# Optimization experiments

Hardware: AMD Instinct MI355X
Metric: run time of the kernel (lower is better)

Reference implementation:

```python
import jax, jax.numpy as jnp
import numpy as np
from jax import lax

D_MODEL, D_STATE, D_CONV, D_INNER, DT_RANK = 1024, 16, 4, 2048, 64
B_SZ, L_SEQ = 2, 4096

def setup_inputs() -> dict:
    key = jax.random.key(0)
    ks = jax.random.split(key, 12)
    s = 0.02
    x = jax.random.normal(ks[0], (B_SZ, L_SEQ, D_MODEL), jnp.float32)
    norm_w = jnp.ones((D_MODEL,), jnp.float32)
    norm_b = jnp.zeros((D_MODEL,), jnp.float32)
    W_in = jax.random.normal(ks[1], (D_MODEL, 2 * D_INNER), jnp.float32) * s
    conv_w = jax.random.normal(ks[2], (D_INNER, 1, D_CONV), jnp.float32) * 0.5
    conv_b = jnp.zeros((D_INNER,), jnp.float32)
    W_x = jax.random.normal(ks[3], (D_INNER, DT_RANK + 2 * D_STATE), jnp.float32) * s
    W_dt = jax.random.normal(ks[4], (DT_RANK, D_INNER), jnp.float32) * s
    # dt bias init as in the torch module: inverse-softplus of dt in [dt_min, dt_max]
    dt_init = jnp.exp(jax.random.uniform(ks[5], (D_INNER,)) * (np.log(0.1) - np.log(0.001)) + np.log(0.001))
    dt_init = jnp.clip(dt_init, 1e-4, None)
    b_dt = dt_init + jnp.log(-jnp.expm1(-dt_init))
    A_log = jnp.log(jnp.broadcast_to(jnp.arange(1, D_STATE + 1, dtype=jnp.float32)[None, :], (D_INNER, D_STATE)))
    D = jnp.ones((D_INNER,), jnp.float32)
    W_out = jax.random.normal(ks[6], (D_INNER, D_MODEL), jnp.float32) * s
    return {"x": x, "norm_w": norm_w, "norm_b": norm_b, "W_in": W_in,
            "conv_w": conv_w, "conv_b": conv_b, "W_x": W_x, "W_dt": W_dt,
            "b_dt": b_dt, "A_log": A_log, "D": D, "W_out": W_out}

def _silu(v):
    return v * jax.nn.sigmoid(v)

def _layernorm(v, w, b, eps=1e-5):
    mu = jnp.mean(v, axis=-1, keepdims=True)
    var = jnp.var(v, axis=-1, keepdims=True)
    return (v - mu) * lax.rsqrt(var + eps) * w + b

def _selective_scan(u, delta, A, Bm, Cm, Dp):
    # u, delta: [B,L,d_inner]; A: [d_inner,N]; Bm, Cm: [B,L,N]; Dp: [d_inner]
    Bb, L, d_inner = u.shape
    N = A.shape[1]

    def step(h, inp):
        dt_t, u_t, B_t, C_t = inp  # [B,d_inner],[B,d_inner],[B,N],[B,N]
        A_bar = jnp.exp(dt_t[..., None] * A)                       # [B,d_inner,N]
        h = A_bar * h + dt_t[..., None] * B_t[:, None, :] * u_t[..., None]
        y = jnp.sum(h * C_t[:, None, :], axis=-1)                  # [B,d_inner]
        return h, y

    h0 = jnp.zeros((Bb, d_inner, N), u.dtype)
    xs = (jnp.swapaxes(delta, 0, 1), jnp.swapaxes(u, 0, 1),
          jnp.swapaxes(Bm, 0, 1), jnp.swapaxes(Cm, 0, 1))
    _, ys = lax.scan(step, h0, xs)          # ys: [L,B,d_inner]
    y = jnp.swapaxes(ys, 0, 1)
    return y + u * Dp[None, None, :]

def reference(x, norm_w, norm_b, W_in, conv_w, conv_b, W_x, W_dt, b_dt, A_log, D, W_out):
    residual = x
    xn = _layernorm(x, norm_w, norm_b)
    xz = xn @ W_in                                      # [B,L,2*d_inner]
    x_ssm, z = jnp.split(xz, 2, axis=-1)
    # depthwise causal conv1d (torch pads both sides then truncates -> left pad)
    xt = jnp.swapaxes(x_ssm, 1, 2)                      # [B,d_inner,L]
    xt = jnp.pad(xt, ((0, 0), (0, 0), (D_CONV - 1, 0)))
    xc = lax.conv_general_dilated(xt, conv_w, window_strides=(1,), padding='VALID',
                                  feature_group_count=D_INNER,
                                  dimension_numbers=('NCH', 'OIH', 'NCH'))
    xc = xc + conv_b[None, :, None]
    x_conv = jnp.swapaxes(_silu(xc), 1, 2)              # [B,L,d_inner]
    x_dbl = x_conv @ W_x                                # [B,L,dt_rank+2N]
    dt_low, B_mat, C_mat = jnp.split(x_dbl, [DT_RANK, DT_RANK + D_STATE], axis=-1)
    delta = jax.nn.softplus(dt_low @ W_dt + b_dt)       # [B,L,d_inner]
    A = -jnp.exp(A_log)
    y = _selective_scan(x_conv, delta, A, B_mat, C_mat, D)
    y = y * _silu(z)
    return residual + y @ W_out
```

## Files before the change

kernel.cpp:

```cpp
#include <hip/hip_runtime.h>

typedef unsigned short u16;
typedef __attribute__((ext_vector_type(8))) __bf16 bf16x8;
typedef __attribute__((ext_vector_type(4))) float f32x4;

#define LSEQ 4096
#define DMODEL 1024
#define DINNER 2048

__device__ __forceinline__ float bf2f(u16 u) {
  union { unsigned u; float f; } v; v.u = ((unsigned)u) << 16; return v.f;
}
__device__ __forceinline__ u16 f2bf(float f) {
  union { float f; unsigned u; } v; v.f = f;
  unsigned r = v.u + 0x7fffu + ((v.u >> 16) & 1u);
  return (u16)(r >> 16);
}
__device__ __forceinline__ void gload_lds16(const void* g, void* l) {
  __builtin_amdgcn_global_load_lds(
      (__attribute__((address_space(1))) void*)(unsigned long long)g,
      (__attribute__((address_space(3))) void*)(unsigned int)(unsigned long long)l,
      16, 0, 0);
}
__device__ __forceinline__ float sigmoidf_(float v) { return 1.f / (1.f + __expf(-v)); }

__device__ __forceinline__ void swz_block(int gx, int& bn, int& bm) {
  int lin = blockIdx.x + gridDim.x * blockIdx.y;
  int q = (gridDim.x * gridDim.y) >> 3;
  int s = (lin & 7) * q + (lin >> 3);
  bn = s % gx;
  bm = s / gx;
}

#define SBAR { __builtin_amdgcn_s_barrier(); __builtin_amdgcn_sched_barrier(0); }

__global__ __launch_bounds__(256) void ln_kernel(const float* __restrict__ x,
                                                 const float* __restrict__ w,
                                                 const float* __restrict__ b,
                                                 u16* __restrict__ out) {
  int row = blockIdx.x;
  const float* xr = x + (size_t)row * DMODEL;
  int t = threadIdx.x;
  float4 v = ((const float4*)xr)[t];
  float s = v.x + v.y + v.z + v.w;
  float s2 = v.x * v.x + v.y * v.y + v.z * v.z + v.w * v.w;
  for (int off = 32; off; off >>= 1) {
    s += __shfl_down(s, off);
    s2 += __shfl_down(s2, off);
  }
  __shared__ float ls[4], ls2[4];
  int wid = t >> 6;
  if ((t & 63) == 0) { ls[wid] = s; ls2[wid] = s2; }
  __syncthreads();
  s = ls[0] + ls[1] + ls[2] + ls[3];
  s2 = ls2[0] + ls2[1] + ls2[2] + ls2[3];
  float mu = s * (1.f / DMODEL);
  float var = s2 * (1.f / DMODEL) - mu * mu;
  float rs = rsqrtf(var + 1e-5f);
  float4 wv = ((const float4*)w)[t];
  float4 bv = ((const float4*)b)[t];
  unsigned p0 = (unsigned)f2bf((v.x - mu) * rs * wv.x + bv.x) |
                ((unsigned)f2bf((v.y - mu) * rs * wv.y + bv.y) << 16);
  unsigned p1 = (unsigned)f2bf((v.z - mu) * rs * wv.z + bv.z) |
                ((unsigned)f2bf((v.w - mu) * rs * wv.w + bv.w) << 16);
  ((uint2*)(out + (size_t)row * DMODEL))[t] = make_uint2(p0, p1);
}

__global__ __launch_bounds__(256) void tc_all(const float* __restrict__ W_in,
                                              const float* __restrict__ W_x,
                                              const float* __restrict__ W_dt,
                                              const float* __restrict__ W_out,
                                              u16* __restrict__ o0, u16* __restrict__ o1,
                                              u16* __restrict__ o2, u16* __restrict__ o3) {
  __shared__ float tile[32][33];
  int id = blockIdx.x;
  const float* in;
  u16* out;
  int K, N, Npad, gx, bx;
  if (id < 4096)      { in = W_in;  out = o0; K = 1024; N = 4096; Npad = 4096; gx = 128; bx = id; }
  else if (id < 4352) { in = W_x;   out = o1; K = 2048; N = 96;   Npad = 128;  gx = 4;   bx = id - 4096; }
  else if (id < 4480) { in = W_dt;  out = o2; K = 64;   N = 2048; Npad = 2048; gx = 64;  bx = id - 4352; }
  else                { in = W_out; out = o3; K = 2048; N = 1024; Npad = 1024; gx = 32;  bx = id - 4480; }
  int n0 = (bx % gx) * 32, k0 = (bx / gx) * 32;
  int tx = threadIdx.x & 31, ty = threadIdx.x >> 5;
  for (int i = ty; i < 32; i += 8) {
    int k = k0 + i, n = n0 + tx;
    tile[i][tx] = (k < K && n < N) ? in[(size_t)k * N + n] : 0.f;
  }
  __syncthreads();
  for (int i = ty; i < 32; i += 8) {
    int n = n0 + i, k = k0 + tx;
    if (n < Npad && k < K) out[(size_t)n * K + k] = f2bf(tile[tx][i]);
  }
}

__device__ __forceinline__ void stage8(const u16* grow0, int ld, int kcol0,
                                       u16* lds_u, int ln) {
  int rr = ln >> 3, kb = ln & 7;
  gload_lds16(grow0 + (size_t)rr * ld + kcol0 + ((kb ^ rr) << 3), lds_u);
}

#define LDA_F(mh, BUF)                                                             \
  _Pragma("unroll") for (int mf = 0; mf < 4; ++mf) {                               \
    av[mf][0] = *(const bf16x8*)(qA0 + (BUF) * 16384 + ((mh) * 64 + mf * 16) * 64); \
    av[mf][1] = *(const bf16x8*)(qA1 + (BUF) * 16384 + ((mh) * 64 + mf * 16) * 64); \
  }

#define LDB_F(nh, BUF)                                                             \
  _Pragma("unroll") for (int nf = 0; nf < 2; ++nf) {                               \
    bb[nh][nf][0] = *(const bf16x8*)(qB0 + (BUF) * 16384 + ((nh) * 32 + nf * 16) * 64); \
    bb[nh][nf][1] = *(const bf16x8*)(qB1 + (BUF) * 16384 + ((nh) * 32 + nf * 16) * 64); \
  }

#define MFMA_Q(mh, nh)                                                             \
  __builtin_amdgcn_s_setprio(1);                                                   \
  _Pragma("unroll") for (int mf = 0; mf < 4; ++mf)                                 \
  _Pragma("unroll") for (int nf = 0; nf < 2; ++nf)                                 \
  _Pragma("unroll") for (int kk = 0; kk < 2; ++kk)                                 \
    acc[(mh) * 4 + mf][(nh) * 2 + nf] = __builtin_amdgcn_mfma_f32_16x16x32_bf16(   \
        av[mf][kk], bb[nh][nf][kk], acc[(mh) * 4 + mf][(nh) * 2 + nf], 0, 0, 0);   \
  __builtin_amdgcn_s_setprio(0);

#define STAGE_A(unit, kt, buf)                                                     \
  _Pragma("unroll") for (int c = 0; c < 2; ++c) {                                  \
    int g = w * 2 + c;                                                             \
    int r0 = ((g < 8) ? g * 8 : (g - 8) * 8 + 128) + (unit) * 64;                  \
    stage8(Ag + (size_t)r0 * ldK, ldK, (kt) * 64, LA + (buf) * 16384 + r0 * 64, ln); \
  }

#define STAGE_B(half, kt, buf)                                                     \
  _Pragma("unroll") for (int c = 0; c < 2; ++c) {                                  \
    int g = w * 2 + c;                                                             \
    int r0 = (g >> 2) * 64 + (half) * 32 + (g & 3) * 8;                            \
    stage8(Bg + (size_t)r0 * ldK, ldK, (kt) * 64, LB + (buf) * 16384 + r0 * 64, ln); \
  }

#define PHASES8P(T_, B0_, B1_)                                                     \
  {                                                                                \
    int kt1 = ((T_) + 1 < NT) ? (T_) + 1 : NT - 1;                                 \
    int kt2 = ((T_) + 2 < NT) ? (T_) + 2 : NT - 1;                                 \
    LDA_F(0, B0_); LDB_F(0, B0_);                                                  \
    STAGE_A(1, kt1, B1_);                                                          \
    MFMA_Q(0, 0);                                                                  \
    SBAR                                                                           \
    LDB_F(1, B0_);                                                                 \
    STAGE_A(0, kt2, B0_);                                                          \
    MFMA_Q(0, 1);                                                                  \
    SBAR                                                                           \
    LDA_F(1, B0_);                                                                 \
    STAGE_B(0, kt2, B0_);                                                          \
    MFMA_Q(1, 1);                                                                  \
    SBAR                                                                           \
    STAGE_B(1, kt2, B0_);                                                          \
    asm volatile("s_waitcnt vmcnt(6)" ::: "memory");                               \
    MFMA_Q(1, 0);                                                                  \
    SBAR                                                                           \
  }

template <int OUT_BF16, int EPI>
__global__ __launch_bounds__(512, 2) void gemm8p(const u16* __restrict__ A,
                                                 const u16* __restrict__ Bt,
                                                 void* __restrict__ Cout,
                                                 const float* __restrict__ aux,
                                                 int M, int N, int K, int cthresh) {
  __shared__ alignas(16) u16 lds[65536];
  u16* LA = lds;
  u16* LB = lds + 32768;
  int t = threadIdx.x;
  int w = t >> 6, ln = t & 63;
  int wm = w >> 2, wn = w & 3;
  int bn, bm;
  swz_block(gridDim.x, bn, bm);
  int lr = ln & 15, lq = ln >> 4, key = ln & 7;
  int ldK = K;
  int NT = K >> 6;
  const u16* Ag = A + (size_t)bm * 256 * ldK;
  const u16* Bg = Bt + (size_t)bn * 256 * ldK;
  const u16* qA0 = LA + (wm * 128 + lr) * 64 + ((lq ^ key) << 3);
  const u16* qA1 = LA + (wm * 128 + lr) * 64 + (((4 + lq) ^ key) << 3);
  const u16* qB0 = LB + (wn * 64 + lr) * 64 + ((lq ^ key) << 3);
  const u16* qB1 = LB + (wn * 64 + lr) * 64 + (((4 + lq) ^ key) << 3);
  f32x4 acc[8][4] = {};
  bf16x8 av[4][2], bb[2][2][2];

  STAGE_A(0, 0, 0); STAGE_B(0, 0, 0); STAGE_B(1, 0, 0); STAGE_A(1, 0, 0);
  int k1 = NT > 1 ? 1 : 0;
  STAGE_A(0, k1, 1); STAGE_B(0, k1, 1); STAGE_B(1, k1, 1);
  asm volatile("s_waitcnt vmcnt(6)" ::: "memory");
  SBAR

  for (int TT = 0; TT < NT; TT += 2) {
    PHASES8P(TT, 0, 1)
    PHASES8P(TT + 1, 1, 0)
  }

  int crow0 = bm * 256 + wm * 128;
  int ccol0 = bn * 256 + wn * 64;
#pragma unroll
  for (int mf = 0; mf < 8; ++mf)
#pragma unroll
    for (int nf = 0; nf < 4; ++nf)
#pragma unroll
      for (int r = 0; r < 4; ++r) {
        int row = crow0 + mf * 16 + lq * 4 + r;
        int col = ccol0 + nf * 16 + lr;
        float v = acc[mf][nf][r];
        if (EPI == 1) v += aux[(size_t)row * N + col];
        if (EPI == 2 && col >= cthresh) v = v * sigmoidf_(v);
        if (OUT_BF16)
          ((u16*)Cout)[(size_t)row * N + col] = f2bf(v);
        else
          ((float*)Cout)[(size_t)row * N + col] = v;
      }
}

#define LDA128(mh, BUF)                                                            \
  _Pragma("unroll") for (int mf2 = 0; mf2 < 2; ++mf2) {                            \
    av[mf2][0] = *(const bf16x8*)(rA0 + (BUF) * 8192 + ((mh) * 32 + mf2 * 16) * 64); \
    av[mf2][1] = *(const bf16x8*)(rA1 + (BUF) * 8192 + ((mh) * 32 + mf2 * 16) * 64); \
  }

#define LDB128(nh, BUF, B_)                                                        \
  _Pragma("unroll") for (int nf2 = 0; nf2 < 2; ++nf2) {                            \
    B_[nf2][0] = *(const bf16x8*)(rB0 + (BUF) * 16384 + ((nh) * 32 + nf2 * 16) * 64); \
    B_[nf2][1] = *(const bf16x8*)(rB1 + (BUF) * 16384 + ((nh) * 32 + nf2 * 16) * 64); \
  }

#define MFMA_Q128(mh, nh, B_)                                                      \
  __builtin_amdgcn_s_setprio(1);                                                   \
  _Pragma("unroll") for (int mf2 = 0; mf2 < 2; ++mf2)                              \
  _Pragma("unroll") for (int nf2 = 0; nf2 < 2; ++nf2)                              \
  _Pragma("unroll") for (int kk = 0; kk < 2; ++kk)                                 \
    acc[(mh) * 2 + mf2][(nh) * 2 + nf2] = __builtin_amdgcn_mfma_f32_16x16x32_bf16( \
        av[mf2][kk], B_[nf2][kk], acc[(mh) * 2 + mf2][(nh) * 2 + nf2], 0, 0, 0);   \
  __builtin_amdgcn_s_setprio(0);

#define STAGE_A128(unit, kt, buf)                                                  \
  {                                                                                \
    int r0 = (w >> 2) * 64 + (unit) * 32 + (w & 3) * 8;                            \
    stage8(Ag + (size_t)r0 * ldK, ldK, (kt) * 64, LA + (buf) * 8192 + r0 * 64, ln); \
  }

#define STAGE_B128(half, kt, buf)                                                  \
  _Pragma("unroll") for (int c = 0; c < 2; ++c) {                                  \
    int g = w * 2 + c;                                                             \
    int r0 = (g >> 2) * 64 + (half) * 32 + (g & 3) * 8;                            \
    stage8(Bg + (size_t)r0 * ldK, ldK, (kt) * 64, LB + (buf) * 16384 + r0 * 64, ln); \
  }

#define PHASES128(T_, B0_, B1_)                                                    \
  {                                                                                \
    int kt1 = ((T_) + 1 < NT) ? (T_) + 1 : NT - 1;                                 \
    int kt2 = ((T_) + 2 < NT) ? (T_) + 2 : NT - 1;                                 \
    LDA128(0, B0_);                                                                \
    LDB128(0, B0_, bbl);                                                           \
    STAGE_A128(1, kt1, B1_);                                                       \
    MFMA_Q128(0, 0, bbl);                                                          \
    SBAR                                                                           \
    LDB128(1, B0_, bbh);                                                           \
    STAGE_A128(0, kt2, B0_);                                                       \
    MFMA_Q128(0, 1, bbh);                                                          \
    SBAR                                                                           \
    LDA128(1, B0_);                                                                \
    STAGE_B128(0, kt2, B0_);                                                       \
    MFMA_Q128(1, 1, bbh);                                                          \
    SBAR                                                                           \
    STAGE_B128(1, kt2, B0_);                                                       \
    asm volatile("s_waitcnt vmcnt(5)" ::: "memory");                               \
    MFMA_Q128(1, 0, bbl);                                                          \
    SBAR                                                                           \
  }

__global__ __launch_bounds__(512, 2) void gemm128_res(const u16* __restrict__ A,
                                                      const u16* __restrict__ Bt,
                                                      float* __restrict__ Cout,
                                                      const float* __restrict__ res,
                                                      int M, int N, int K) {
  __shared__ alignas(16) u16 lds[49152];
  u16* LA = lds;
  u16* LB = lds + 16384;
  int t = threadIdx.x;
  int w = t >> 6, ln = t & 63;
  int wm = w >> 2, wn = w & 3;
  int bn, bm;
  swz_block(gridDim.x, bn, bm);
  int lr = ln & 15, lq = ln >> 4, key = ln & 7;
  int ldK = K;
  int NT = K >> 6;
  const u16* Ag = A + (size_t)bm * 128 * ldK;
  const u16* Bg = Bt + (size_t)bn * 256 * ldK;
  const u16* rA0 = LA + (wm * 64 + lr) * 64 + ((lq ^ key) << 3);
  const u16* rA1 = LA + (wm * 64 + lr) * 64 + (((4 + lq) ^ key) << 3);
  const u16* rB0 = LB + (wn * 64 + lr) * 64 + ((lq ^ key) << 3);
  const u16* rB1 = LB + (wn * 64 + lr) * 64 + (((4 + lq) ^ key) << 3);
  f32x4 acc[4][4] = {};
  bf16x8 av[2][2], bbl[2][2], bbh[2][2];

  STAGE_A128(0, 0, 0); STAGE_B128(0, 0, 0); STAGE_B128(1, 0, 0); STAGE_A128(1, 0, 0);
  int k1 = NT > 1 ? 1 : 0;
  STAGE_A128(0, k1, 1); STAGE_B128(0, k1, 1); STAGE_B128(1, k1, 1);
  asm volatile("s_waitcnt vmcnt(5)" ::: "memory");
  SBAR

  for (int TT = 0; TT < NT; TT += 2) {
    PHASES128(TT, 0, 1)
    PHASES128(TT + 1, 1, 0)
  }

  int crow0 = bm * 128 + wm * 64;
  int ccol0 = bn * 256 + wn * 64;
#pragma unroll
  for (int mf = 0; mf < 4; ++mf)
#pragma unroll
    for (int nf = 0; nf < 4; ++nf)
#pragma unroll
      for (int r = 0; r < 4; ++r) {
        int row = crow0 + mf * 16 + lq * 4 + r;
        int col = ccol0 + nf * 16 + lr;
        Cout[(size_t)row * N + col] = acc[mf][nf][r] + res[(size_t)row * N + col];
      }
}

template <int OUT_BF16, int EPI, int SPLITK>
__global__ __launch_bounds__(256) void gemm_bt(const u16* __restrict__ A,
                                               const u16* __restrict__ Bt,
                                               void* __restrict__ Cout,
                                               const float* __restrict__ aux,
                                               int M, int N, int K, int ld, int cthresh) {
  __shared__ alignas(16) u16 As[128 * 32];
  __shared__ alignas(16) u16 Bs[128 * 32];
  int t = threadIdx.x;
  int w = t >> 6, ln = t & 63;
  int wr = w >> 1, wc = w & 1;
  int bm = blockIdx.y, bn = blockIdx.x;
  int lr = ln & 15, lk = (ln >> 4) * 8;
  f32x4 acc[4][4] = {};
  int kz = SPLITK ? blockIdx.z * K : 0;
  const u16* Abase = A + (size_t)bm * 128 * ld + kz;
  const u16* Bbase = Bt + (size_t)bn * 128 * ld + kz;
  for (int k0 = 0; k0 < K; k0 += 32) {
#pragma unroll
    for (int c = 0; c < 2; ++c) {
      int chunk = w * 2 + c;
      int ee = chunk * 512 + ln * 8;
      int row = ee >> 5, col = ee & 31;
      gload_lds16(Abase + (size_t)row * ld + k0 + col, As + chunk * 512);
      gload_lds16(Bbase + (size_t)row * ld + k0 + col, Bs + chunk * 512);
    }
    __syncthreads();
    bf16x8 af[4], bfr[4];
#pragma unroll
    for (int m = 0; m < 4; ++m)
      af[m] = *(const bf16x8*)(As + (wr * 64 + m * 16 + lr) * 32 + lk);
#pragma unroll
    for (int n = 0; n < 4; ++n)
      bfr[n] = *(const bf16x8*)(Bs + (wc * 64 + n * 16 + lr) * 32 + lk);
#pragma unroll
    for (int m = 0; m < 4; ++m)
#pragma unroll
      for (int n = 0; n < 4; ++n)
        acc[m][n] = __builtin_amdgcn_mfma_f32_16x16x32_bf16(af[m], bfr[n], acc[m][n], 0, 0, 0);
    __syncthreads();
  }
  int rb = bm * 128 + wr * 64 + (ln >> 4) * 4;
  int cb = bn * 128 + wc * 64 + lr;
  float* Cpart = SPLITK ? ((float*)Cout + (size_t)blockIdx.z * M * N) : (float*)Cout;
#pragma unroll
  for (int m = 0; m < 4; ++m)
#pragma unroll
    for (int n = 0; n < 4; ++n)
#pragma unroll
      for (int r = 0; r < 4; ++r) {
        int row = rb + m * 16 + r;
        int col = cb + n * 16;
        float v = acc[m][n][r];
        if (EPI == 3) {
          float dtr = v + aux[col];
          v = dtr > 15.f ? dtr : __logf(1.f + __expf(dtr));
        }
        if (OUT_BF16)
          ((u16*)Cpart)[(size_t)row * N + col] = f2bf(v);
        else
          Cpart[(size_t)row * N + col] = v;
      }
}

__global__ __launch_bounds__(256) void reduce_xdbl(const float* __restrict__ part,
                                                   float* __restrict__ xdbl,
                                                   u16* __restrict__ dtlow) {
  int i = blockIdx.x * 256 + threadIdx.x;
  float s = 0.f;
#pragma unroll
  for (int z = 0; z < 8; ++z) s += part[(size_t)z * (8192 * 128) + i];
  xdbl[i] = s;
  int col = i & 127;
  if (col < 64) dtlow[(size_t)(i >> 7) * 64 + col] = f2bf(s);
}

__global__ __launch_bounds__(256) void conv_silu(const u16* __restrict__ xz,
                                                 const float* __restrict__ cw,
                                                 const float* __restrict__ cb,
                                                 u16* __restrict__ out) {
  int d2 = blockIdx.x * 256 + threadIdx.x;
  int d = d2 * 2;
  int l0 = blockIdx.y * 8;
  int b = blockIdx.z;
  float w0a = cw[d * 4 + 0], w1a = cw[d * 4 + 1], w2a = cw[d * 4 + 2], w3a = cw[d * 4 + 3];
  float w0b = cw[d * 4 + 4], w1b = cw[d * 4 + 5], w2b = cw[d * 4 + 6], w3b = cw[d * 4 + 7];
  float biasa = cb[d], biasb = cb[d + 1];
  const u16* xp = xz + ((size_t)b * LSEQ) * 4096 + d;
  float xa[11], xb[11];
#pragma unroll
  for (int i = 0; i < 11; ++i) {
    int l = l0 - 3 + i;
    unsigned pk = (l >= 0) ? *(const unsigned*)(xp + (size_t)l * 4096) : 0u;
    xa[i] = bf2f((u16)(pk & 0xffffu));
    xb[i] = bf2f((u16)(pk >> 16));
  }
  u16* op = out + ((size_t)b * LSEQ + l0) * DINNER + d;
#pragma unroll
  for (int i = 0; i < 8; ++i) {
    float va = biasa + w0a * xa[i] + w1a * xa[i + 1] + w2a * xa[i + 2] + w3a * xa[i + 3];
    float vb = biasb + w0b * xb[i] + w1b * xb[i + 1] + w2b * xb[i + 2] + w3b * xb[i + 3];
    unsigned pk = (unsigned)f2bf(va * sigmoidf_(va)) |
                  ((unsigned)f2bf(vb * sigmoidf_(vb)) << 16);
    *(unsigned*)(op + (size_t)i * DINNER) = pk;
  }
}

__device__ __forceinline__ void compute_a(float dt, const float* An, bool fast, float* av) {
  if (fast) {
    float q = __expf(-dt);
    float q2 = q * q, q4 = q2 * q2;
    av[0] = q; av[1] = q2; av[2] = q2 * q; av[3] = q4;
#pragma unroll
    for (int n = 4; n < 16; ++n) av[n] = av[n - 4] * q4;
  } else {
#pragma unroll
    for (int n = 0; n < 16; ++n) av[n] = __expf(dt * An[n]);
  }
}

__device__ __forceinline__ void load_An(const float* A_log, int d, float* An, bool& fast) {
  const float4* A4 = (const float4*)(A_log + (size_t)d * 16);
  fast = true;
#pragma unroll
  for (int q = 0; q < 4; ++q) {
    float4 a = A4[q];
    An[q * 4 + 0] = -__expf(a.x);
    An[q * 4 + 1] = -__expf(a.y);
    An[q * 4 + 2] = -__expf(a.z);
    An[q * 4 + 3] = -__expf(a.w);
  }
#pragma unroll
  for (int n = 0; n < 16; ++n)
    fast = fast && (__builtin_fabsf(An[n] + (float)(n + 1)) < 1e-3f * (n + 1));
}

__global__ __launch_bounds__(256) void scan1(const u16* __restrict__ dtbf,
                                             const u16* __restrict__ ubf,
                                             const float* __restrict__ xdbl,
                                             const float* __restrict__ A_log,
                                             float* __restrict__ P,
                                             float* __restrict__ H) {
  int d = blockIdx.x * 256 + threadIdx.x;
  int b = blockIdx.y, c = blockIdx.z;
  size_t row0 = (size_t)b * LSEQ + c * 64;
  float An[16];
  bool fast;
  load_An(A_log, d, An, fast);
  const u16* dtp = dtbf + row0 * DINNER + d;
  const u16* up = ubf + row0 * DINNER + d;
  const float* Bp = xdbl + row0 * 128 + 64;
  float h[16];
#pragma unroll
  for (int n = 0; n < 16; ++n) h[n] = 0.f;
  float sdt = 0.f;
  float dt_c = bf2f(dtp[0]);
  float uu_c = bf2f(up[0]);
  const float4* B4 = (const float4*)Bp;
  float4 b0c = B4[0], b1c = B4[1], b2c = B4[2], b3c = B4[3];
  for (int i = 0; i < 64; ++i) {
    float dt_n = dt_c, uu_n = uu_c;
    float4 b0n = b0c, b1n = b1c, b2n = b2c, b3n = b3c;
    if (i < 63) {
      dt_n = bf2f(dtp[(size_t)(i + 1) * DINNER]);
      uu_n = bf2f(up[(size_t)(i + 1) * DINNER]);
      const float4* B4n = (const float4*)(Bp + (size_t)(i + 1) * 128);
      b0n = B4n[0]; b1n = B4n[1]; b2n = B4n[2]; b3n = B4n[3];
    }
    float dtu = dt_c * uu_c;
    sdt += dt_c;
    float Bf[16] = {b0c.x, b0c.y, b0c.z, b0c.w, b1c.x, b1c.y, b1c.z, b1c.w,
                    b2c.x, b2c.y, b2c.z, b2c.w, b3c.x, b3c.y, b3c.z, b3c.w};
    float av[16];
    compute_a(dt_c, An, fast, av);
#pragma unroll
    for (int n = 0; n < 16; ++n) h[n] = av[n] * h[n] + dtu * Bf[n];
    dt_c = dt_n; uu_c = uu_n;
    b0c = b0n; b1c = b1n; b2c = b2n; b3c = b3n;
  }
  size_t idx = (size_t)c * 65536 + ((size_t)b * DINNER + d) * 16;
  float4* P4 = (float4*)(P + idx);
  float4* H4 = (float4*)(H + idx);
#pragma unroll
  for (int q = 0; q < 4; ++q) {
    P4[q] = make_float4(__expf(An[q * 4 + 0] * sdt), __expf(An[q * 4 + 1] * sdt),
                        __expf(An[q * 4 + 2] * sdt), __expf(An[q * 4 + 3] * sdt));
    H4[q] = make_float4(h[q * 4], h[q * 4 + 1], h[q * 4 + 2], h[q * 4 + 3]);
  }
}

__global__ __launch_bounds__(256) void scan2(const float* __restrict__ P,
                                             const float* __restrict__ H,
                                             float* __restrict__ Hinit) {
  int i = blockIdx.x * 256 + threadIdx.x;
  float h = 0.f;
  for (int c = 0; c < 64; ++c) {
    Hinit[(size_t)c * 65536 + i] = h;
    h = P[(size_t)c * 65536 + i] * h + H[(size_t)c * 65536 + i];
  }
}

__global__ __launch_bounds__(256) void scan3(const u16* __restrict__ dtbf,
                                             const u16* __restrict__ ubf,
                                             const float* __restrict__ xdbl,
                                             const float* __restrict__ A_log,
                                             const float* __restrict__ Dp,
                                             const u16* __restrict__ xzbf,
                                             const float* __restrict__ Hinit,
                                             u16* __restrict__ ybf) {
  int d = blockIdx.x * 256 + threadIdx.x;
  int b = blockIdx.y, c = blockIdx.z;
  size_t row0 = (size_t)b * LSEQ + c * 64;
  float An[16];
  bool fast;
  load_An(A_log, d, An, fast);
  const u16* dtp = dtbf + row0 * DINNER + d;
  const u16* up = ubf + row0 * DINNER + d;
  const float* Bp = xdbl + row0 * 128 + 64;
  const float* Cp = xdbl + row0 * 128 + 80;
  const u16* gp = xzbf + row0 * 4096 + DINNER + d;
  u16* yp = ybf + row0 * DINNER + d;
  float Dv = Dp[d];
  float h[16];
  {
    const float4* Hi4 = (const float4*)(Hinit + (size_t)c * 65536 + ((size_t)b * DINNER + d) * 16);
#pragma unroll
    for (int q = 0; q < 4; ++q) {
      float4 hv = Hi4[q];
      h[q * 4 + 0] = hv.x; h[q * 4 + 1] = hv.y; h[q * 4 + 2] = hv.z; h[q * 4 + 3] = hv.w;
    }
  }
  float dt_c = bf2f(dtp[0]);
  float uu_c = bf2f(up[0]);
  float g_c = bf2f(gp[0]);
  const float4* B4 = (const float4*)Bp;
  const float4* C4 = (const float4*)Cp;
  float4 b0c = B4[0], b1c = B4[1], b2c = B4[2], b3c = B4[3];
  float4 c0c = C4[0], c1c = C4[1], c2c = C4[2], c3c = C4[3];
  for (int i = 0; i < 64; ++i) {
    float dt_n = dt_c, uu_n = uu_c, g_n = g_c;
    float4 b0n = b0c, b1n = b1c, b2n = b2c, b3n = b3c;
    float4 c0n = c0c, c1n = c1c, c2n = c2c, c3n = c3c;
    if (i < 63) {
      dt_n = bf2f(dtp[(size_t)(i + 1) * DINNER]);
      uu_n = bf2f(up[(size_t)(i + 1) * DINNER]);
      g_n = bf2f(gp[(size_t)(i + 1) * 4096]);
      const float4* B4n = (const float4*)(Bp + (size_t)(i + 1) * 128);
      const float4* C4n = (const float4*)(Cp + (size_t)(i + 1) * 128);
      b0n = B4n[0]; b1n = B4n[1]; b2n = B4n[2]; b3n = B4n[3];
      c0n = C4n[0]; c1n = C4n[1]; c2n = C4n[2]; c3n = C4n[3];
    }
    float dtu = dt_c * uu_c;
    float Bf[16] = {b0c.x, b0c.y, b0c.z, b0c.w, b1c.x, b1c.y, b1c.z, b1c.w,
                    b2c.x, b2c.y, b2c.z, b2c.w, b3c.x, b3c.y, b3c.z, b3c.w};
    float Cf[16] = {c0c.x, c0c.y, c0c.z, c0c.w, c1c.x, c1c.y, c1c.z, c1c.w,
                    c2c.x, c2c.y, c2c.z, c2c.w, c3c.x, c3c.y, c3c.z, c3c.w};
    float av[16];
    compute_a(dt_c, An, fast, av);
    float y = 0.f;
#pragma unroll
    for (int n = 0; n < 16; ++n) {
      h[n] = av[n] * h[n] + dtu * Bf[n];
      y += h[n] * Cf[n];
    }
    yp[(size_t)i * DINNER] = f2bf((y + uu_c * Dv) * g_c);
    dt_c = dt_n; uu_c = uu_n; g_c = g_n;
    b0c = b0n; b1c = b1n; b2c = b2n; b3c = b3n;
    c0c = c0n; c1c = c1n; c2c = c2n; c3c = c3n;
  }
}

extern "C" void kernel_launch(void* const* d_in, const int* in_sizes, int n_in,
                              void* d_out, int out_size, void* d_ws, size_t ws_size,
                              hipStream_t stream) {
  const float* x = (const float*)d_in[0];
  const float* nw = (const float*)d_in[1];
  const float* nb = (const float*)d_in[2];
  const float* W_in = (const float*)d_in[3];
  const float* convw = (const float*)d_in[4];
  const float* convb = (const float*)d_in[5];
  const float* W_x = (const float*)d_in[6];
  const float* W_dt = (const float*)d_in[7];
  const float* b_dt = (const float*)d_in[8];
  const float* A_log = (const float*)d_in[9];
  const float* Dp = (const float*)d_in[10];
  const float* W_out = (const float*)d_in[11];
  float* out = (float*)d_out;

  char* wp = (char*)d_ws;
  auto alloc = [&](size_t bytes) {
    char* p = wp;
    wp += (bytes + 255) & ~(size_t)255;
    return p;
  };
  u16* xz_bf = (u16*)alloc((size_t)8192 * 4096 * 2);
  u16* xconv_bf = (u16*)alloc((size_t)8192 * 2048 * 2);
  u16* xn_bf = (u16*)alloc((size_t)8192 * 1024 * 2);
  float* xdbl = (float*)alloc((size_t)8192 * 128 * 4);
  u16* dt_bf = (u16*)alloc((size_t)8192 * 2048 * 2);
  u16* dtlow_bf = (u16*)alloc((size_t)8192 * 64 * 2);
  u16* Wint = (u16*)alloc((size_t)4096 * 1024 * 2);
  u16* Wxt = (u16*)alloc((size_t)128 * 2048 * 2);
  u16* Wdtt = (u16*)alloc((size_t)2048 * 64 * 2);
  u16* Woutt = (u16*)alloc((size_t)1024 * 2048 * 2);
  float* P = (float*)alloc((size_t)64 * 65536 * 4);
  float* H = (float*)alloc((size_t)64 * 65536 * 4);
  float* Hinit = (float*)alloc((size_t)64 * 65536 * 4);
  float* xdbl_part = (float*)P;
  u16* y_bf = (u16*)P;

  tc_all<<<6528, 256, 0, stream>>>(W_in, W_x, W_dt, W_out, Wint, Wxt, Wdtt, Woutt);

  ln_kernel<<<8192, 256, 0, stream>>>(x, nw, nb, xn_bf);
  gemm8p<1, 2><<<dim3(16, 32), 512, 0, stream>>>(xn_bf, Wint, xz_bf, nullptr,
                                                 8192, 4096, 1024, 2048);
  conv_silu<<<dim3(4, 512, 2), 256, 0, stream>>>(xz_bf, convw, convb, xconv_bf);
  gemm_bt<0, 0, 1><<<dim3(1, 64, 8), 256, 0, stream>>>(xconv_bf, Wxt, xdbl_part, nullptr,
                                                       8192, 128, 256, 2048, 0);
  reduce_xdbl<<<4096, 256, 0, stream>>>(xdbl_part, xdbl, dtlow_bf);
  gemm_bt<1, 3, 0><<<dim3(16, 64), 256, 0, stream>>>(dtlow_bf, Wdtt, dt_bf, b_dt,
                                                     8192, 2048, 64, 64, 0);
  scan1<<<dim3(8, 2, 64), 256, 0, stream>>>(dt_bf, xconv_bf, xdbl, A_log, P, H);
  scan2<<<256, 256, 0, stream>>>(P, H, Hinit);
  scan3<<<dim3(8, 2, 64), 256, 0, stream>>>(dt_bf, xconv_bf, xdbl, A_log, Dp, xz_bf,
                                            Hinit, y_bf);
  gemm128_res<<<dim3(4, 64), 512, 0, stream>>>(y_bf, Woutt, out, x, 8192, 1024, 2048);
}
```

Before: 311.2 us.

## Merge weight transpose with layernorm launch and halve GEMM main-loop barriers

Folds the weight-transpose kernel and the layernorm kernel into one launch, with block index selecting the role, so one launch gap disappears and both can fill the GPU together. In the two pipelined bf16 GEMMs, each k-step phase sequence is regrouped from four barriers to two: both B fragments are loaded up front, all next-tile global-to-LDS staging is issued together, and two MFMA quarters run between each pair of barriers. This cuts barrier stalls but raises register pressure, and it changes the order of LDS staging relative to fragment reads, which risks hazards on the shared buffer.

```diff
diff --git a/kernel.cpp b/kernel.cpp
--- a/kernel.cpp
+++ b/kernel.cpp
@@ -34,46 +34,47 @@
 
 #define SBAR { __builtin_amdgcn_s_barrier(); __builtin_amdgcn_sched_barrier(0); }
 
-__global__ __launch_bounds__(256) void ln_kernel(const float* __restrict__ x,
-                                                 const float* __restrict__ w,
-                                                 const float* __restrict__ b,
-                                                 u16* __restrict__ out) {
-  int row = blockIdx.x;
-  const float* xr = x + (size_t)row * DMODEL;
+__global__ __launch_bounds__(256) void tc_ln_all(const float* __restrict__ W_in,
+                                                 const float* __restrict__ W_x,
+                                                 const float* __restrict__ W_dt,
+                                                 const float* __restrict__ W_out,
+                                                 u16* __restrict__ o0, u16* __restrict__ o1,
+                                                 u16* __restrict__ o2, u16* __restrict__ o3,
+                                                 const float* __restrict__ x,
+                                                 const float* __restrict__ nw,
+                                                 const float* __restrict__ nb,
+                                                 u16* __restrict__ xn_out) {
+  int id = blockIdx.x;
   int t = threadIdx.x;
-  float4 v = ((const float4*)xr)[t];
-  float s = v.x + v.y + v.z + v.w;
-  float s2 = v.x * v.x + v.y * v.y + v.z * v.z + v.w * v.w;
-  for (int off = 32; off; off >>= 1) {
-    s += __shfl_down(s, off);
-    s2 += __shfl_down(s2, off);
-  }
-  __shared__ float ls[4], ls2[4];
-  int wid = t >> 6;
-  if ((t & 63) == 0) { ls[wid] = s; ls2[wid] = s2; }
-  __syncthreads();
-  s = ls[0] + ls[1] + ls[2] + ls[3];
-  s2 = ls2[0] + ls2[1] + ls2[2] + ls2[3];
-  float mu = s * (1.f / DMODEL);
-  float var = s2 * (1.f / DMODEL) - mu * mu;
-  float rs = rsqrtf(var + 1e-5f);
-  float4 wv = ((const float4*)w)[t];
-  float4 bv = ((const float4*)b)[t];
-  unsigned p0 = (unsigned)f2bf((v.x - mu) * rs * wv.x + bv.x) |
-                ((unsigned)f2bf((v.y - mu) * rs * wv.y + bv.y) << 16);
-  unsigned p1 = (unsigned)f2bf((v.z - mu) * rs * wv.z + bv.z) |
-                ((unsigned)f2bf((v.w - mu) * rs * wv.w + bv.w) << 16);
-  ((uint2*)(out + (size_t)row * DMODEL))[t] = make_uint2(p0, p1);
-}
-
-__global__ __launch_bounds__(256) void tc_all(const float* __restrict__ W_in,
-                                              const float* __restrict__ W_x,
-                                              const float* __restrict__ W_dt,
-                                              const float* __restrict__ W_out,
-                                              u16* __restrict__ o0, u16* __restrict__ o1,
-                                              u16* __restrict__ o2, u16* __restrict__ o3) {
+  if (id >= 6528) {
+    int row = id - 6528;
+    const float* xr = x + (size_t)row * DMODEL;
+    float4 v = ((const float4*)xr)[t];
+    float s = v.x + v.y + v.z + v.w;
+    float s2 = v.x * v.x + v.y * v.y + v.z * v.z + v.w * v.w;
+    for (int off = 32; off; off >>= 1) {
+      s += __shfl_down(s, off);
+      s2 += __shfl_down(s2, off);
+    }
+    __shared__ float ls[4], ls2[4];
+    int wid = t >> 6;
+    if ((t & 63) == 0) { ls[wid] = s; ls2[wid] = s2; }
+    __syncthreads();
+    s = ls[0] + ls[1] + ls[2] + ls[3];
+    s2 = ls2[0] + ls2[1] + ls2[2] + ls2[3];
+    float mu = s * (1.f / DMODEL);
+    float var = s2 * (1.f / DMODEL) - mu * mu;
+    float rs = rsqrtf(var + 1e-5f);
+    float4 wv = ((const float4*)nw)[t];
+    float4 bv = ((const float4*)nb)[t];
+    unsigned p0 = (unsigned)f2bf((v.x - mu) * rs * wv.x + bv.x) |
+                  ((unsigned)f2bf((v.y - mu) * rs * wv.y + bv.y) << 16);
+    unsigned p1 = (unsigned)f2bf((v.z - mu) * rs * wv.z + bv.z) |
+                  ((unsigned)f2bf((v.w - mu) * rs * wv.w + bv.w) << 16);
+    ((uint2*)(xn_out + (size_t)row * DMODEL))[t] = make_uint2(p0, p1);
+    return;
+  }
   __shared__ float tile[32][33];
-  int id = blockIdx.x;
   const float* in;
   u16* out;
   int K, N, Npad, gx, bx;
@@ -82,7 +83,7 @@
   else if (id < 4480) { in = W_dt;  out = o2; K = 64;   N = 2048; Npad = 2048; gx = 64;  bx = id - 4352; }
   else                { in = W_out; out = o3; K = 2048; N = 1024; Npad = 1024; gx = 32;  bx = id - 4480; }
   int n0 = (bx % gx) * 32, k0 = (bx / gx) * 32;
-  int tx = threadIdx.x & 31, ty = threadIdx.x >> 5;
+  int tx = t & 31, ty = t >> 5;
   for (int i = ty; i < 32; i += 8) {
     int k = k0 + i, n = n0 + tx;
     tile[i][tx] = (k < K && n < N) ? in[(size_t)k * N + n] : 0.f;
@@ -139,20 +140,17 @@
   {                                                                                \
     int kt1 = ((T_) + 1 < NT) ? (T_) + 1 : NT - 1;                                 \
     int kt2 = ((T_) + 2 < NT) ? (T_) + 2 : NT - 1;                                 \
-    LDA_F(0, B0_); LDB_F(0, B0_);                                                  \
+    LDA_F(0, B0_); LDB_F(0, B0_); LDB_F(1, B0_);                                   \
     STAGE_A(1, kt1, B1_);                                                          \
     MFMA_Q(0, 0);                                                                  \
-    SBAR                                                                           \
-    LDB_F(1, B0_);                                                                 \
-    STAGE_A(0, kt2, B0_);                                                          \
     MFMA_Q(0, 1);                                                                  \
     SBAR                                                                           \
     LDA_F(1, B0_);                                                                 \
+    STAGE_A(0, kt2, B0_);                                                          \
     STAGE_B(0, kt2, B0_);                                                          \
-    MFMA_Q(1, 1);                                                                  \
-    SBAR                                                                           \
     STAGE_B(1, kt2, B0_);                                                          \
     asm volatile("s_waitcnt vmcnt(6)" ::: "memory");                               \
+    MFMA_Q(1, 1);                                                                  \
     MFMA_Q(1, 0);                                                                  \
     SBAR                                                                           \
   }
@@ -254,19 +252,17 @@
     int kt2 = ((T_) + 2 < NT) ? (T_) + 2 : NT - 1;                                 \
     LDA128(0, B0_);                                                                \
     LDB128(0, B0_, bbl);                                                           \
+    LDB128(1, B0_, bbh);                                                           \
     STAGE_A128(1, kt1, B1_);                                                       \
     MFMA_Q128(0, 0, bbl);                                                          \
-    SBAR                                                                           \
-    LDB128(1, B0_, bbh);                                                           \
-    STAGE_A128(0, kt2, B0_);                                                       \
     MFMA_Q128(0, 1, bbh);                                                          \
     SBAR                                                                           \
     LDA128(1, B0_);                                                                \
+    STAGE_A128(0, kt2, B0_);                                                       \
     STAGE_B128(0, kt2, B0_);                                                       \
-    MFMA_Q128(1, 1, bbh);                                                          \
-    SBAR                                                                           \
     STAGE_B128(1, kt2, B0_);                                                       \
     asm volatile("s_waitcnt vmcnt(5)" ::: "memory");                               \
+    MFMA_Q128(1, 1, bbh);                                                          \
     MFMA_Q128(1, 0, bbl);                                                          \
     SBAR                                                                           \
   }
@@ -631,9 +627,9 @@
   float* xdbl_part = (float*)P;
   u16* y_bf = (u16*)P;
 
-  tc_all<<<6528, 256, 0, stream>>>(W_in, W_x, W_dt, W_out, Wint, Wxt, Wdtt, Woutt);
-
-  ln_kernel<<<8192, 256, 0, stream>>>(x, nw, nb, xn_bf);
+  tc_ln_all<<<6528 + 8192, 256, 0, stream>>>(W_in, W_x, W_dt, W_out, Wint, Wxt, Wdtt, Woutt,
+                                             x, nw, nb, xn_bf);
+
   gemm8p<1, 2><<<dim3(16, 32), 512, 0, stream>>>(xn_bf, Wint, xz_bf, nullptr,
                                                  8192, 4096, 1024, 2048);
   conv_silu<<<dim3(4, 512, 2), 256, 0, stream>>>(xz_bf, convw, convb, xconv_bf);
```

Result: no change. 306.1 us (-1.6%).
